# Performance work log

Measured on AMD Instinct MI355X. Metric: run time of the kernel, lower is better.

The kernel has to match this reference:

```python
import jax, jax.numpy as jnp
import numpy as np

B, TOK, D, H, L = 64, 20, 512, 8, 4
S = 512          # tokens per half
HD = D // H
ODIM = 32        # encoder_output_dim


def _ln(x, g, b):
    m = x.mean(-1, keepdims=True)
    v = ((x - m) ** 2).mean(-1, keepdims=True)
    return (x - m) / jnp.sqrt(v + 1e-5) * g + b


def _alibi_slopes(h):
    # mirrors FlashAttentionBlock.build_alibi_slopes (base=2.0)
    base = 2.0
    return jnp.asarray([1.0 / base ** (i // (h // base)) for i in range(h)], dtype=jnp.float32)


def setup_inputs() -> dict:
    key = jax.random.key(0)
    ks = jax.random.split(key, 16)
    r = lambda i, shape, s=0.02: jax.random.normal(ks[i], shape, jnp.float32) * s
    return {
        'x': jax.random.normal(ks[0], (B, 2 * S * TOK), jnp.float32),
        'in_W': r(1, (TOK, D)), 'in_b': jnp.zeros((D,)),
        'qkv_W': r(2, (L, D, 3 * D)), 'qkv_b': jnp.zeros((L, 3 * D)),
        'ln1_g': jnp.ones((L, D)), 'ln1_b': jnp.zeros((L, D)),
        'ffn_W1': r(3, (L, D, 4 * D)), 'ffn_b1': jnp.zeros((L, 4 * D)),
        'ffn_W2': r(4, (L, 4 * D, D)), 'ffn_b2': jnp.zeros((L, D)),
        'ln2_g': jnp.ones((L, D)), 'ln2_b': jnp.zeros((L, D)),
        'out_W': r(5, (D, ODIM)), 'out_b': jnp.zeros((ODIM,)),
        'd1_W': r(6, (2 * S * ODIM, 256)), 'd1_b': jnp.zeros((256,)),
        'bn1_g': jnp.ones((256,)), 'bn1_b': jnp.zeros((256,)),
        'bn1_m': jnp.zeros((256,)), 'bn1_v': jnp.ones((256,)),
        'd2_W': r(7, (256, 128)), 'd2_b': jnp.zeros((128,)),
        'bn2_g': jnp.ones((128,)), 'bn2_b': jnp.zeros((128,)),
        'bn2_m': jnp.zeros((128,)), 'bn2_v': jnp.ones((128,)),
        'fin_W': r(8, (128, 1)), 'fin_b': jnp.zeros((1,)),
    }


def _forward(x, in_W, in_b, qkv_W, qkv_b, ln1_g, ln1_b, ffn_W1, ffn_b1,
             ffn_W2, ffn_b2, ln2_g, ln2_b, out_W, out_b,
             d1_W, d1_b, bn1_g, bn1_b, bn1_m, bn1_v,
             d2_W, d2_b, bn2_g, bn2_b, bn2_m, bn2_v, fin_W, fin_b):
    slopes = _alibi_slopes(H)                                   # [H]
    pos = jnp.arange(S)
    # non-causal ALiBi bias: -slope * |i - j|, shape [H, S, S]
    bias = -slopes[:, None, None] * jnp.abs(pos[:, None] - pos[None, :]).astype(jnp.float32)
    scale = 1.0 / np.sqrt(HD).astype(np.float32)

    def encode(xh):
        b = xh.shape[0]
        t = xh.reshape(b, S, TOK) @ in_W + in_b                 # [b, S, D]
        for l in range(L):
            res = t
            qkv = (t @ qkv_W[l] + qkv_b[l]).reshape(b, S, 3, H, HD)
            q, k, v = qkv[:, :, 0], qkv[:, :, 1], qkv[:, :, 2]  # [b, S, H, HD]
            scores = jnp.einsum('bqhd,bkhd->bhqk', q, k) * scale + bias[None]
            attn = jax.nn.softmax(scores, axis=-1)
            o = jnp.einsum('bhqk,bkhd->bqhd', attn, v).reshape(b, S, D)
            t = _ln(res + o, ln1_g[l], ln1_b[l])
            res = t
            f = jax.nn.relu(t @ ffn_W1[l] + ffn_b1[l]) @ ffn_W2[l] + ffn_b2[l]
            t = _ln(res + f, ln2_g[l], ln2_b[l])
        return (t @ out_W + out_b).reshape(b, -1)               # [b, S*ODIM]

    half = S * TOK
    h = jnp.concatenate([encode(x[:, :half]), encode(x[:, half:])], axis=-1)
    bn = lambda z, g, bb, m, v: (z - m) / jnp.sqrt(v + 1e-5) * g + bb
    h = bn(jax.nn.relu(h @ d1_W + d1_b), bn1_g, bn1_b, bn1_m, bn1_v)
    h = bn(jax.nn.relu(h @ d2_W + d2_b), bn2_g, bn2_b, bn2_m, bn2_v)
    return (h @ fin_W + fin_b).squeeze(-1)                      # [B]


def reference(x, in_W, in_b, qkv_W, qkv_b, ln1_g, ln1_b, ffn_W1, ffn_b1,
              ffn_W2, ffn_b2, ln2_g, ln2_b, out_W, out_b,
              d1_W, d1_b, bn1_g, bn1_b, bn1_m, bn1_v,
              d2_W, d2_b, bn2_g, bn2_b, bn2_m, bn2_v, fin_W, fin_b):
    return _forward(x, in_W, in_b, qkv_W, qkv_b, ln1_g, ln1_b, ffn_W1, ffn_b1,
                    ffn_W2, ffn_b2, ln2_g, ln2_b, out_W, out_b,
                    d1_W, d1_b, bn1_g, bn1_b, bn1_m, bn1_v,
                    d2_W, d2_b, bn2_g, bn2_b, bn2_m, bn2_v, fin_W, fin_b)
```

## Files before the change

kernel.cpp:

```cpp
#include <hip/hip_runtime.h>

#define DEV __device__ __forceinline__

using bf16x8 = __attribute__((ext_vector_type(8))) __bf16;
using f32x4  = __attribute__((ext_vector_type(4))) float;
using u16x8  = __attribute__((ext_vector_type(8))) unsigned short;
using u16x4  = __attribute__((ext_vector_type(4))) unsigned short;

DEV unsigned short f2bf(float f) {
  unsigned u = __builtin_bit_cast(unsigned, f);
  u += 0x7fffu + ((u >> 16) & 1u);
  return (unsigned short)(u >> 16);
}
DEV float bf2f(unsigned short h) {
  unsigned u = ((unsigned)h) << 16;
  return __builtin_bit_cast(float, u);
}
DEV f32x4 mfma16(u16x8 a, u16x8 b, f32x4 c) {
  return __builtin_amdgcn_mfma_f32_16x16x32_bf16(
      __builtin_bit_cast(bf16x8, a), __builtin_bit_cast(bf16x8, b), c, 0, 0, 0);
}
DEV f32x4 zero4() { f32x4 z = {0.f, 0.f, 0.f, 0.f}; return z; }

DEV void glds16(const unsigned short* g, unsigned short* l) {
  __builtin_amdgcn_global_load_lds(
      (const __attribute__((address_space(1))) unsigned int*)g,
      (__attribute__((address_space(3))) unsigned int*)l, 16, 0, 0);
}

enum { EPI_BIAS = 0, EPI_RELU = 1, EPI_OUT = 2 };

template <int EPI>
__global__ __launch_bounds__(512, 2) void gemm256_k(
    const unsigned short* __restrict__ A, const unsigned short* __restrict__ Bt,
    const float* __restrict__ bias, unsigned short* __restrict__ C, int N, int K) {
  __shared__ unsigned short As[2][8192];
  __shared__ unsigned short Bs[2][8192];
  const int tid = threadIdx.x;
  const int lane = tid & 63, wv = tid >> 6;
  const int q = lane >> 4, ln = lane & 15;
  const int wr = wv >> 2, wc = wv & 3;

  const int Nt = gridDim.x, Mt = gridDim.y;
  const int lin = blockIdx.x + Nt * blockIdx.y;
  const int xcd = lin & 7;
  const int j = lin >> 3;
  const int mi = xcd * (Mt >> 3) + j / Nt;
  const int ni = j % Nt;
  const int m0 = mi << 8, n0 = ni << 8;

  f32x4 acc[8][4];
#pragma unroll
  for (int i = 0; i < 8; ++i)
#pragma unroll
    for (int jj = 0; jj < 4; ++jj) acc[i][jj] = zero4();

  const int srow = wv * 16 + (lane >> 2);
  const int scol = (((lane & 3) ^ ((lane >> 3) & 3)) << 3);
  const unsigned short* Ap = A + (size_t)(m0 + srow) * K + scol;
  const unsigned short* Bp = Bt + (size_t)(n0 + srow) * K + scol;

  auto STAGE = [&](int buf, int kb) {
    unsigned short* ab = &As[buf][wv * 512];
    unsigned short* bb = &Bs[buf][wv * 512];
    glds16(Ap + kb, ab);
    glds16(Ap + (size_t)128 * K + kb, ab + 4096);
    glds16(Bp + kb, bb);
    glds16(Bp + (size_t)128 * K + kb, bb + 4096);
  };

  const int sw = ((q ^ ((ln >> 1) & 3)) << 3);
  const int NTt = K >> 5;

  STAGE(0, 0);
  if (NTt > 1) {
    STAGE(1, 32);
    asm volatile("s_waitcnt vmcnt(4)" ::: "memory");
  } else {
    asm volatile("s_waitcnt vmcnt(0)" ::: "memory");
  }
  __builtin_amdgcn_sched_barrier(0);
  __builtin_amdgcn_s_barrier();
  __builtin_amdgcn_sched_barrier(0);

  for (int t = 0; t < NTt; ++t) {
    const int cur = t & 1;
    u16x8 af[4], bf[4], ag[4];
#pragma unroll
    for (int mt = 0; mt < 4; ++mt)
      af[mt] = *(const u16x8*)(&As[cur][(wr * 128 + mt * 16 + ln) * 32 + sw]);
#pragma unroll
    for (int nt = 0; nt < 4; ++nt)
      bf[nt] = *(const u16x8*)(&Bs[cur][(wc * 64 + nt * 16 + ln) * 32 + sw]);
    __builtin_amdgcn_s_setprio(1);
#pragma unroll
    for (int nt = 0; nt < 4; ++nt)
#pragma unroll
      for (int mt = 0; mt < 4; ++mt) acc[mt][nt] = mfma16(af[mt], bf[nt], acc[mt][nt]);
    __builtin_amdgcn_s_setprio(0);
#pragma unroll
    for (int mt = 0; mt < 4; ++mt)
      ag[mt] = *(const u16x8*)(&As[cur][(wr * 128 + (mt + 4) * 16 + ln) * 32 + sw]);
    asm volatile("s_waitcnt lgkmcnt(0)" ::: "memory");
    __builtin_amdgcn_sched_barrier(0);
    __builtin_amdgcn_s_barrier();
    __builtin_amdgcn_sched_barrier(0);
    if (t + 2 < NTt) STAGE(cur, (t + 2) * 32);
    __builtin_amdgcn_s_setprio(1);
#pragma unroll
    for (int nt = 0; nt < 4; ++nt)
#pragma unroll
      for (int mt = 0; mt < 4; ++mt)
        acc[mt + 4][nt] = mfma16(ag[mt], bf[nt], acc[mt + 4][nt]);
    __builtin_amdgcn_s_setprio(0);
    if (t < NTt - 1) {
      if (t + 2 < NTt) {
        asm volatile("s_waitcnt vmcnt(4)" ::: "memory");
      } else {
        asm volatile("s_waitcnt vmcnt(0)" ::: "memory");
      }
      __builtin_amdgcn_sched_barrier(0);
      __builtin_amdgcn_s_barrier();
      __builtin_amdgcn_sched_barrier(0);
    }
  }

#pragma unroll
  for (int mt = 0; mt < 8; ++mt) {
    const int rowb = m0 + wr * 128 + mt * 16 + q * 4;
#pragma unroll
    for (int nt = 0; nt < 4; ++nt) {
      const int col = n0 + wc * 64 + nt * 16 + ln;
      const float bs = bias[col];
#pragma unroll
      for (int r = 0; r < 4; ++r) {
        float v = acc[mt][nt][r] + bs;
        if (EPI == EPI_RELU) v = fmaxf(v, 0.f);
        C[(size_t)(rowb + r) * N + col] = f2bf(v);
      }
    }
  }
}

template <int EPI>
__global__ __launch_bounds__(256) void gemm_k(
    const unsigned short* __restrict__ A, const unsigned short* __restrict__ Bt,
    const float* __restrict__ bias, unsigned short* __restrict__ C, int N, int K) {
  __shared__ unsigned short As[128 * 64];
  __shared__ unsigned short Bs[128 * 64];
  const int tid = threadIdx.x;
  const int lane = tid & 63, wv = tid >> 6;
  const int q = lane >> 4, ln = lane & 15;
  const int wr = wv >> 1, wc = wv & 1;

  const int Nt = gridDim.x, Mt = gridDim.y;
  const int lin = blockIdx.x + Nt * blockIdx.y;
  const int xcd = lin & 7;
  const int j = lin >> 3;
  const int mi = xcd * (Mt >> 3) + j / Nt;
  const int ni = j % Nt;
  const int m0 = mi << 7, n0 = ni << 7;

  f32x4 acc[4][4];
#pragma unroll
  for (int i = 0; i < 4; ++i)
#pragma unroll
    for (int jj = 0; jj < 4; ++jj) acc[i][jj] = zero4();

  const int ra = lane >> 3;
  const int ca = ((lane & 7) ^ ra) << 3;
  const unsigned short* Ap = A + (size_t)(m0 + wv * 32 + ra) * K + ca;
  const unsigned short* Bp = Bt + (size_t)(n0 + wv * 32 + ra) * K + ca;
  unsigned short* AsW = As + wv * 2048;
  unsigned short* BsW = Bs + wv * 2048;
  const int ln7 = ln & 7;

  for (int kb = 0; kb < K; kb += 64) {
    __syncthreads();
#pragma unroll
    for (int t = 0; t < 4; ++t) {
      glds16(Ap + (size_t)(t * 8) * K + kb, AsW + t * 512);
      glds16(Bp + (size_t)(t * 8) * K + kb, BsW + t * 512);
    }
    __syncthreads();
#pragma unroll
    for (int kk = 0; kk < 2; ++kk) {
      const int c = kk * 4 + q;
      const int lo = ln * 64 + ((c ^ ln7) << 3);
      u16x8 af[4];
#pragma unroll
      for (int mt = 0; mt < 4; ++mt)
        af[mt] = *(const u16x8*)(As + (wr * 64 + mt * 16) * 64 + lo);
#pragma unroll
      for (int nt = 0; nt < 4; ++nt) {
        u16x8 bf = *(const u16x8*)(Bs + (wc * 64 + nt * 16) * 64 + lo);
#pragma unroll
        for (int mt = 0; mt < 4; ++mt) acc[mt][nt] = mfma16(af[mt], bf, acc[mt][nt]);
      }
    }
  }

#pragma unroll
  for (int mt = 0; mt < 4; ++mt) {
    const int rowb = m0 + wr * 64 + mt * 16 + q * 4;
#pragma unroll
    for (int nt = 0; nt < 4; ++nt) {
      const int col = n0 + wc * 64 + nt * 16 + ln;
      if (EPI == EPI_OUT && col >= 32) continue;
      const float bs = bias[col];
      const int ldc = (EPI == EPI_OUT) ? 32 : N;
#pragma unroll
      for (int r = 0; r < 4; ++r) {
        float v = acc[mt][nt][r] + bs;
        if (EPI == EPI_RELU) v = fmaxf(v, 0.f);
        C[(size_t)(rowb + r) * ldc + col] = f2bf(v);
      }
    }
  }
}

__global__ __launch_bounds__(256) void vt_k(const unsigned short* __restrict__ big,
                                            unsigned short* __restrict__ vt) {
  __shared__ unsigned short td[64 * 72];
  const int tid = threadIdx.x;
  const int sh = blockIdx.x;
  const int seq = sh >> 3, h = sh & 7;
  const int kt = blockIdx.y;
  {
    const int key = tid >> 2, hdc = (tid & 3) << 4;
    const unsigned short* src =
        big + ((size_t)seq * 512 + kt * 64 + key) * 1536 + 1024 + h * 64 + hdc;
    *(u16x8*)(td + key * 72 + hdc) = *(const u16x8*)src;
    *(u16x8*)(td + key * 72 + hdc + 8) = *(const u16x8*)(src + 8);
  }
  __syncthreads();
  {
    const int hd = tid >> 2, kc = (tid & 3) << 4;
    u16x8 a, b;
#pragma unroll
    for (int j = 0; j < 8; ++j) a[j] = td[(kc + j) * 72 + hd];
#pragma unroll
    for (int j = 0; j < 8; ++j) b[j] = td[(kc + 8 + j) * 72 + hd];
    unsigned short* dst = vt + ((size_t)sh * 64 + hd) * 512 + kt * 64 + kc;
    *(u16x8*)dst = a;
    *(u16x8*)(dst + 8) = b;
  }
}

__global__ __launch_bounds__(256) void attn_k(const unsigned short* __restrict__ qkv,
                                              const unsigned short* __restrict__ vt,
                                              unsigned short* __restrict__ o) {
  __shared__ unsigned short Qs[128 * 72];
  __shared__ unsigned short Ks[64 * 64];
  __shared__ unsigned short Vts[64 * 64];
  unsigned short* Ps = Qs;
  const int tid = threadIdx.x;
  const int lane = tid & 63, w = tid >> 6, q = lane >> 4, ln = lane & 15;
  const int bh = blockIdx.x;
  const int seq = bh >> 3, h = bh & 7;
  const int qt = blockIdx.y;
  const size_t tokb = (size_t)seq * 512;
  const int qoff = h * 64, koff = 512 + h * 64;
  const float c1 = 0.125f * 1.44269504f;
  const float c2 = ((h < 4) ? 1.0f : 0.5f) * 1.44269504f;

#pragma unroll
  for (int p = 0; p < 4; ++p) {
    int c = p * 256 + tid;
    int row = c >> 3, cc = (c & 7) << 3;
    u16x8 v = *(const u16x8*)(qkv + (tokb + qt * 128 + row) * 1536 + qoff + cc);
    *(u16x8*)(Qs + row * 72 + cc) = v;
  }
  __syncthreads();
  u16x8 aq[2][2];
#pragma unroll
  for (int mt = 0; mt < 2; ++mt)
#pragma unroll
    for (int kc = 0; kc < 2; ++kc)
      aq[mt][kc] = *(const u16x8*)(Qs + (w * 32 + mt * 16 + ln) * 72 + kc * 32 + q * 8);

  float lacc[2] = {0.f, 0.f};
  f32x4 o_acc[2][4];
#pragma unroll
  for (int mt = 0; mt < 2; ++mt)
#pragma unroll
    for (int ht = 0; ht < 4; ++ht) o_acc[mt][ht] = zero4();

  const int sr = lane >> 3;
  const int sc = ((lane & 7) ^ sr) << 3;
  const unsigned short* Kp = qkv + (tokb + w * 16 + sr) * 1536 + koff + sc;
  const unsigned short* Vp = vt + ((size_t)bh * 64 + w * 16 + sr) * 512 + sc;
  unsigned short* KsW = Ks + w * 1024;
  unsigned short* VsW = Vts + w * 1024;
  const int ln7 = ln & 7;

  for (int kt = 0; kt < 8; ++kt) {
    __syncthreads();
    glds16(Kp + (size_t)(kt * 64) * 1536, KsW);
    glds16(Kp + (size_t)(kt * 64 + 8) * 1536, KsW + 512);
    glds16(Vp + kt * 64, VsW);
    glds16(Vp + kt * 64 + (size_t)8 * 512, VsW + 512);
    __syncthreads();

    f32x4 sacc[2][4];
#pragma unroll
    for (int mt = 0; mt < 2; ++mt)
#pragma unroll
      for (int nt = 0; nt < 4; ++nt) sacc[mt][nt] = zero4();
#pragma unroll
    for (int nt = 0; nt < 4; ++nt)
#pragma unroll
      for (int kc = 0; kc < 2; ++kc) {
        u16x8 bk = *(const u16x8*)(Ks + (nt * 16 + ln) * 64 + (((kc * 4 + q) ^ ln7) << 3));
#pragma unroll
        for (int mt = 0; mt < 2; ++mt) sacc[mt][nt] = mfma16(bk, aq[mt][kc], sacc[mt][nt]);
      }

    const float qp0 = (float)(qt * 128 + w * 32 + ln);
    const float kb0 = (float)(kt * 64 + q * 4);
#pragma unroll
    for (int mt = 0; mt < 2; ++mt) {
      const float qpm = qp0 + (float)(mt * 16);
#pragma unroll
      for (int nt = 0; nt < 4; ++nt) {
        const float kp = kb0 + (float)(nt * 16);
        u16x4 pk;
#pragma unroll
        for (int r = 0; r < 4; ++r) {
          const float ad = fabsf(qpm - (kp + (float)r));
          const float p = exp2f(fmaf(sacc[mt][nt][r], c1, -c2 * ad));
          const unsigned u = __builtin_bit_cast(unsigned, p);
          const unsigned short pb = (unsigned short)((u + 0x8000u) >> 16);
          pk[r] = pb;
          lacc[mt] += bf2f(pb);
        }
        *(u16x4*)(Ps + (w * 32 + mt * 16 + ln) * 72 + nt * 16 + q * 4) = pk;
      }
    }
#pragma unroll
    for (int kc = 0; kc < 2; ++kc) {
      u16x8 pa[2];
#pragma unroll
      for (int mt = 0; mt < 2; ++mt)
        pa[mt] = *(const u16x8*)(Ps + (w * 32 + mt * 16 + ln) * 72 + kc * 32 + q * 8);
#pragma unroll
      for (int ht = 0; ht < 4; ++ht) {
        u16x8 bv = *(const u16x8*)(Vts + (ht * 16 + ln) * 64 + (((kc * 4 + q) ^ ln7) << 3));
#pragma unroll
        for (int mt = 0; mt < 2; ++mt) o_acc[mt][ht] = mfma16(pa[mt], bv, o_acc[mt][ht]);
      }
    }
  }

  float rl[2][4];
#pragma unroll
  for (int mt = 0; mt < 2; ++mt) {
    float l = lacc[mt];
    l += __shfl_xor(l, 16, 64);
    l += __shfl_xor(l, 32, 64);
    const int sb = (lane >> 4) * 20;
#pragma unroll
    for (int r = 0; r < 4; ++r) rl[mt][r] = 1.0f / __shfl(l, sb + r, 64);
  }

#pragma unroll
  for (int mt = 0; mt < 2; ++mt)
#pragma unroll
    for (int ht = 0; ht < 4; ++ht)
#pragma unroll
      for (int r = 0; r < 4; ++r) {
        const int row = qt * 128 + w * 32 + mt * 16 + q * 4 + r;
        const float val = o_acc[mt][ht][r] * rl[mt][r];
        o[(tokb + row) * 512 + h * 64 + ht * 16 + ln] = f2bf(val);
      }
}

__global__ __launch_bounds__(256) void ln_k(const unsigned short* res,
                                            const unsigned short* __restrict__ y,
                                            const float* __restrict__ g,
                                            const float* __restrict__ b,
                                            unsigned short* out) {
  const int lane = threadIdx.x & 63, wv = threadIdx.x >> 6;
  const size_t row = (size_t)blockIdx.x * 4 + wv;
  const size_t base = row * 512 + lane * 8;
  u16x8 rv = *(const u16x8*)(res + base);
  u16x8 yv = *(const u16x8*)(y + base);
  float v[8];
  float s = 0.f, s2 = 0.f;
#pragma unroll
  for (int i = 0; i < 8; ++i) {
    v[i] = bf2f(rv[i]) + bf2f(yv[i]);
    s += v[i];
    s2 += v[i] * v[i];
  }
#pragma unroll
  for (int m = 1; m < 64; m <<= 1) {
    s += __shfl_xor(s, m, 64);
    s2 += __shfl_xor(s2, m, 64);
  }
  const float mean = s * (1.f / 512.f);
  const float var = s2 * (1.f / 512.f) - mean * mean;
  const float rstd = rsqrtf(var + 1e-5f);
  const int c = lane * 8;
  u16x8 ov;
#pragma unroll
  for (int i = 0; i < 8; ++i) ov[i] = f2bf((v[i] - mean) * rstd * g[c + i] + b[c + i]);
  *(u16x8*)(out + base) = ov;
}

__global__ __launch_bounds__(256) void transpose_w(const float* __restrict__ in,
                                                   unsigned short* __restrict__ out,
                                                   int Kin, int Nin, int Kout, int Nout) {
  __shared__ float tile[32][33];
  const int nb = blockIdx.x * 32, kb = blockIdx.y * 32;
  const int tx = threadIdx.x & 31, ty = threadIdx.x >> 5;
#pragma unroll
  for (int i = 0; i < 32; i += 8) {
    int k = kb + ty + i, n = nb + tx;
    tile[ty + i][tx] = (k < Kin && n < Nin) ? in[(size_t)k * Nin + n] : 0.f;
  }
  __syncthreads();
#pragma unroll
  for (int i = 0; i < 32; i += 8) {
    int n = nb + ty + i, k = kb + tx;
    if (n < Nout && k < Kout) out[(size_t)n * Kout + k] = f2bf(tile[tx][ty + i]);
  }
}

__global__ __launch_bounds__(256) void xpad_k(const float* __restrict__ x,
                                              unsigned short* __restrict__ xp) {
  const int idx = blockIdx.x * 256 + threadIdx.x;
  const int tok = idx >> 6, k = idx & 63;
  const int seq = tok >> 9, s = tok & 511;
  const int hf = seq >> 6, b = seq & 63;
  float v = 0.f;
  if (k < 20) v = x[(size_t)b * 20480 + hf * 10240 + s * 20 + k];
  xp[idx] = f2bf(v);
}

__global__ __launch_bounds__(256) void d1_part(const unsigned short* __restrict__ enc,
                                               const float* __restrict__ W,
                                               float* __restrict__ pz) {
  __shared__ float ef[64 * 128];
  const int tid = threadIdx.x;
  const int kb = blockIdx.x * 128;
  const int hf = kb >> 14;
  const int j0 = kb & 16383;
  {
    const int m = tid >> 2, c = (tid & 3) * 32;
    const unsigned short* src = enc + (size_t)hf * 1048576 + (size_t)m * 16384 + j0 + c;
#pragma unroll
    for (int i = 0; i < 4; ++i) {
      u16x8 v = *(const u16x8*)(src + i * 8);
#pragma unroll
      for (int jj = 0; jj < 8; ++jj) ef[m * 128 + c + i * 8 + jj] = bf2f(v[jj]);
    }
  }
  __syncthreads();
  const int n = tid;
  float acc[64];
#pragma unroll
  for (int m = 0; m < 64; ++m) acc[m] = 0.f;
  for (int kc = 0; kc < 128; kc += 4) {
    const float w0 = W[(size_t)(kb + kc) * 256 + n];
    const float w1 = W[(size_t)(kb + kc + 1) * 256 + n];
    const float w2 = W[(size_t)(kb + kc + 2) * 256 + n];
    const float w3 = W[(size_t)(kb + kc + 3) * 256 + n];
#pragma unroll
    for (int m = 0; m < 64; ++m) {
      const f32x4 e = *(const f32x4*)(ef + m * 128 + kc);
      acc[m] += e[0] * w0 + e[1] * w1 + e[2] * w2 + e[3] * w3;
    }
  }
#pragma unroll
  for (int m = 0; m < 64; ++m)
    pz[(size_t)(blockIdx.x * 64 + m) * 256 + n] = acc[m];
}

__global__ __launch_bounds__(256) void d1_fin(const float* __restrict__ pz,
                                              const float* __restrict__ d1b,
                                              const float* __restrict__ g,
                                              const float* __restrict__ b,
                                              const float* __restrict__ mm,
                                              const float* __restrict__ vv,
                                              float* __restrict__ h1) {
  const int m = blockIdx.x, n = threadIdx.x;
  float a = d1b[n];
  for (int sl = 0; sl < 256; ++sl) a += pz[(size_t)(sl * 64 + m) * 256 + n];
  a = fmaxf(a, 0.f);
  a = (a - mm[n]) * rsqrtf(vv[n] + 1e-5f) * g[n] + b[n];
  h1[m * 256 + n] = a;
}

__global__ __launch_bounds__(128) void d2_k(const float* __restrict__ h1,
                                            const float* __restrict__ W,
                                            const float* __restrict__ bb,
                                            const float* __restrict__ g,
                                            const float* __restrict__ b,
                                            const float* __restrict__ mm,
                                            const float* __restrict__ vv,
                                            float* __restrict__ h2) {
  __shared__ float hs[256];
  const int m = blockIdx.x, n = threadIdx.x;
  hs[n] = h1[m * 256 + n];
  hs[n + 128] = h1[m * 256 + n + 128];
  __syncthreads();
  float a = bb[n];
#pragma unroll 8
  for (int k = 0; k < 256; ++k) a += hs[k] * W[k * 128 + n];
  a = fmaxf(a, 0.f);
  a = (a - mm[n]) * rsqrtf(vv[n] + 1e-5f) * g[n] + b[n];
  h2[m * 128 + n] = a;
}

__global__ __launch_bounds__(64) void fin_k(const float* __restrict__ h2,
                                            const float* __restrict__ W,
                                            const float* __restrict__ fb,
                                            float* __restrict__ out) {
  const int m = threadIdx.x;
  float a = fb[0];
#pragma unroll 8
  for (int k = 0; k < 128; ++k) a += h2[m * 128 + k] * W[k];
  out[m] = a;
}

extern "C" void kernel_launch(void* const* d_in, const int* in_sizes, int n_in,
                              void* d_out, int out_size, void* d_ws, size_t ws_size,
                              hipStream_t stream) {
  const float* x      = (const float*)d_in[0];
  const float* in_W   = (const float*)d_in[1];
  const float* in_b   = (const float*)d_in[2];
  const float* qkv_W  = (const float*)d_in[3];
  const float* qkv_b  = (const float*)d_in[4];
  const float* ln1_g  = (const float*)d_in[5];
  const float* ln1_b  = (const float*)d_in[6];
  const float* ffn_W1 = (const float*)d_in[7];
  const float* ffn_b1 = (const float*)d_in[8];
  const float* ffn_W2 = (const float*)d_in[9];
  const float* ffn_b2 = (const float*)d_in[10];
  const float* ln2_g  = (const float*)d_in[11];
  const float* ln2_b  = (const float*)d_in[12];
  const float* out_W  = (const float*)d_in[13];
  const float* out_b  = (const float*)d_in[14];
  const float* d1W    = (const float*)d_in[15];
  const float* d1b    = (const float*)d_in[16];
  const float* bn1g   = (const float*)d_in[17];
  const float* bn1b   = (const float*)d_in[18];
  const float* bn1m   = (const float*)d_in[19];
  const float* bn1v   = (const float*)d_in[20];
  const float* d2W    = (const float*)d_in[21];
  const float* d2b    = (const float*)d_in[22];
  const float* bn2g   = (const float*)d_in[23];
  const float* bn2b   = (const float*)d_in[24];
  const float* bn2m   = (const float*)d_in[25];
  const float* bn2v   = (const float*)d_in[26];
  const float* finW   = (const float*)d_in[27];
  const float* finb   = (const float*)d_in[28];
  (void)in_sizes; (void)n_in; (void)out_size; (void)ws_size;

  char* ws = (char*)d_ws;
  size_t off = 0;
  auto alloc = [&](size_t bytes) {
    char* p = ws + off;
    off += (bytes + 255) & ~(size_t)255;
    return p;
  };
  unsigned short* t     = (unsigned short*)alloc(32768ull * 512 * 2);
  unsigned short* big   = (unsigned short*)alloc(32768ull * 2048 * 2);
  unsigned short* ob    = (unsigned short*)alloc(32768ull * 512 * 2);
  unsigned short* xpad  = (unsigned short*)alloc(65536ull * 64 * 2);
  unsigned short* enc   = (unsigned short*)alloc(65536ull * 32 * 2);
  unsigned short* inWt  = (unsigned short*)alloc(512ull * 64 * 2);
  unsigned short* qkvWt = (unsigned short*)alloc(4ull * 1536 * 512 * 2);
  unsigned short* f1Wt  = (unsigned short*)alloc(4ull * 2048 * 512 * 2);
  unsigned short* f2Wt  = (unsigned short*)alloc(4ull * 512 * 2048 * 2);
  unsigned short* outWt = (unsigned short*)alloc(128ull * 512 * 2);
  float* h1 = (float*)alloc(64ull * 256 * 4);
  float* h2 = (float*)alloc(64ull * 128 * 4);
  float* pz = (float*)big;
  unsigned short* vtb = big + (size_t)32768 * 1536;

  xpad_k<<<16384, 256, 0, stream>>>(x, xpad);
  transpose_w<<<dim3(16, 2), 256, 0, stream>>>(in_W, inWt, 20, 512, 64, 512);
  transpose_w<<<dim3(4, 16), 256, 0, stream>>>(out_W, outWt, 512, 32, 512, 128);
  for (int l = 0; l < 4; ++l) {
    transpose_w<<<dim3(48, 16), 256, 0, stream>>>(qkv_W + (size_t)l * 512 * 1536,
                                                  qkvWt + (size_t)l * 1536 * 512, 512, 1536, 512, 1536);
    transpose_w<<<dim3(64, 16), 256, 0, stream>>>(ffn_W1 + (size_t)l * 512 * 2048,
                                                  f1Wt + (size_t)l * 2048 * 512, 512, 2048, 512, 2048);
    transpose_w<<<dim3(16, 64), 256, 0, stream>>>(ffn_W2 + (size_t)l * 2048 * 512,
                                                  f2Wt + (size_t)l * 512 * 2048, 2048, 512, 2048, 512);
  }

  for (int hf = 0; hf < 2; ++hf) {
    gemm256_k<EPI_BIAS><<<dim3(2, 128), 512, 0, stream>>>(xpad + (size_t)hf * 32768 * 64, inWt, in_b, t, 512, 64);
    for (int l = 0; l < 4; ++l) {
      gemm256_k<EPI_BIAS><<<dim3(6, 128), 512, 0, stream>>>(t, qkvWt + (size_t)l * 1536 * 512,
                                                            qkv_b + l * 1536, big, 1536, 512);
      vt_k<<<dim3(512, 8), 256, 0, stream>>>(big, vtb);
      attn_k<<<dim3(512, 4), 256, 0, stream>>>(big, vtb, ob);
      ln_k<<<8192, 256, 0, stream>>>(t, ob, ln1_g + l * 512, ln1_b + l * 512, t);
      gemm256_k<EPI_RELU><<<dim3(8, 128), 512, 0, stream>>>(t, f1Wt + (size_t)l * 2048 * 512,
                                                            ffn_b1 + l * 2048, big, 2048, 512);
      gemm256_k<EPI_BIAS><<<dim3(2, 128), 512, 0, stream>>>(big, f2Wt + (size_t)l * 512 * 2048,
                                                            ffn_b2 + l * 512, ob, 512, 2048);
      ln_k<<<8192, 256, 0, stream>>>(t, ob, ln2_g + l * 512, ln2_b + l * 512, t);
    }
    gemm_k<EPI_OUT><<<dim3(1, 256), 256, 0, stream>>>(t, outWt, out_b,
                                                      enc + (size_t)hf * 32768 * 32, 128, 512);
  }

  d1_part<<<256, 256, 0, stream>>>(enc, d1W, pz);
  d1_fin<<<64, 256, 0, stream>>>(pz, d1b, bn1g, bn1b, bn1m, bn1v, h1);
  d2_k<<<64, 128, 0, stream>>>(h1, d2W, d2b, bn2g, bn2b, bn2m, bn2v, h2);
  fin_k<<<1, 64, 0, stream>>>(h2, finW, finb, (float*)d_out);
}
```

Before: 3.226 ms.

## Restructure 256x256 GEMM into 8-phase schedule with 64-wide K tiles

Replaces the 256x256 bf16 GEMM main loop with a version that loads 64-wide K tiles into doubled LDS buffers, using an 8-column XOR swizzle. Each K step is split into four MFMA quadrants, and the global-to-LDS loads for the next tiles are interleaved between them, separated by barriers. The goal is to overlap memory traffic with MFMA work and halve the number of loop iterations. In exchange, LDS use doubles, which drops the kernel to one block per CU, and each iteration now has more barriers.

```diff
diff --git a/kernel.cpp b/kernel.cpp
--- a/kernel.cpp
+++ b/kernel.cpp
@@ -28,18 +28,26 @@
       (__attribute__((address_space(3))) unsigned int*)l, 16, 0, 0);
 }
 
+#define PH_BAR()                          \
+  do {                                    \
+    __builtin_amdgcn_sched_barrier(0);    \
+    __builtin_amdgcn_s_barrier();         \
+    __builtin_amdgcn_sched_barrier(0);    \
+  } while (0)
+
 enum { EPI_BIAS = 0, EPI_RELU = 1, EPI_OUT = 2 };
 
 template <int EPI>
-__global__ __launch_bounds__(512, 2) void gemm256_k(
+__global__ __launch_bounds__(512, 1) void gemm8p_k(
     const unsigned short* __restrict__ A, const unsigned short* __restrict__ Bt,
     const float* __restrict__ bias, unsigned short* __restrict__ C, int N, int K) {
-  __shared__ unsigned short As[2][8192];
-  __shared__ unsigned short Bs[2][8192];
+  __shared__ unsigned short As[2][16384];
+  __shared__ unsigned short Bs[2][16384];
   const int tid = threadIdx.x;
   const int lane = tid & 63, wv = tid >> 6;
   const int q = lane >> 4, ln = lane & 15;
   const int wr = wv >> 2, wc = wv & 3;
+  const int ln7 = ln & 7;
 
   const int Nt = gridDim.x, Mt = gridDim.y;
   const int lin = blockIdx.x + Nt * blockIdx.y;
@@ -55,73 +63,126 @@
 #pragma unroll
     for (int jj = 0; jj < 4; ++jj) acc[i][jj] = zero4();
 
-  const int srow = wv * 16 + (lane >> 2);
-  const int scol = (((lane & 3) ^ ((lane >> 3) & 3)) << 3);
-  const unsigned short* Ap = A + (size_t)(m0 + srow) * K + scol;
-  const unsigned short* Bp = Bt + (size_t)(n0 + srow) * K + scol;
-
-  auto STAGE = [&](int buf, int kb) {
-    unsigned short* ab = &As[buf][wv * 512];
-    unsigned short* bb = &Bs[buf][wv * 512];
-    glds16(Ap + kb, ab);
-    glds16(Ap + (size_t)128 * K + kb, ab + 4096);
-    glds16(Bp + kb, bb);
-    glds16(Bp + (size_t)128 * K + kb, bb + 4096);
+  const int sr = lane >> 3;
+  const int sc = ((lane & 7) ^ sr) << 3;
+  const unsigned short* Abase = A + (size_t)(m0 + wv * 8 + sr) * K + sc;
+  const unsigned short* Bbase = Bt + (size_t)(n0 + wv * 8 + sr) * K + sc;
+
+  const int T = K >> 6;
+
+  auto stA = [&](int buf, int t, int half) {
+    unsigned short* d = &As[buf][(half * 128 + wv * 8) * 64];
+    const unsigned short* s = Abase + (size_t)(half * 128) * K + t * 64;
+    glds16(s, d);
+    glds16(s + (size_t)64 * K, d + 4096);
   };
-
-  const int sw = ((q ^ ((ln >> 1) & 3)) << 3);
-  const int NTt = K >> 5;
-
-  STAGE(0, 0);
-  if (NTt > 1) {
-    STAGE(1, 32);
+  auto stB = [&](int buf, int t, int half) {
+    unsigned short* d = &Bs[buf][(half * 128 + wv * 8) * 64];
+    const unsigned short* s = Bbase + (size_t)(half * 128) * K + t * 64;
+    glds16(s, d);
+    glds16(s + (size_t)64 * K, d + 4096);
+  };
+
+  stB(0, 0, 0);
+  stB(0, 0, 1);
+  stA(0, 0, 0);
+  stA(0, 0, 1);
+  if (T > 1) {
+    stB(1, 1, 0);
+    stB(1, 1, 1);
     asm volatile("s_waitcnt vmcnt(4)" ::: "memory");
   } else {
     asm volatile("s_waitcnt vmcnt(0)" ::: "memory");
   }
-  __builtin_amdgcn_sched_barrier(0);
-  __builtin_amdgcn_s_barrier();
-  __builtin_amdgcn_sched_barrier(0);
-
-  for (int t = 0; t < NTt; ++t) {
-    const int cur = t & 1;
-    u16x8 af[4], bf[4], ag[4];
+  PH_BAR();
+
+  for (int u = 0; u < T; ++u) {
+    const int cur = u & 1, nxt = cur ^ 1;
+    const unsigned short* Ab = &As[cur][0];
+    const unsigned short* Bb = &Bs[cur][0];
+    u16x8 a0[4][2], a1[4][2], b0[2][2], b1[2][2];
+
 #pragma unroll
     for (int mt = 0; mt < 4; ++mt)
-      af[mt] = *(const u16x8*)(&As[cur][(wr * 128 + mt * 16 + ln) * 32 + sw]);
-#pragma unroll
-    for (int nt = 0; nt < 4; ++nt)
-      bf[nt] = *(const u16x8*)(&Bs[cur][(wc * 64 + nt * 16 + ln) * 32 + sw]);
+#pragma unroll
+      for (int kk = 0; kk < 2; ++kk)
+        a0[mt][kk] = *(const u16x8*)(Ab + (wr * 128 + mt * 16 + ln) * 64 +
+                                     (((kk * 4 + q) ^ ln7) << 3));
+#pragma unroll
+    for (int nt = 0; nt < 2; ++nt)
+#pragma unroll
+      for (int kk = 0; kk < 2; ++kk)
+        b0[nt][kk] = *(const u16x8*)(Bb + (wc * 64 + nt * 16 + ln) * 64 +
+                                     (((kk * 4 + q) ^ ln7) << 3));
+    if (u + 1 < T) stA(nxt, u + 1, 0);
+    PH_BAR();
     __builtin_amdgcn_s_setprio(1);
 #pragma unroll
-    for (int nt = 0; nt < 4; ++nt)
-#pragma unroll
-      for (int mt = 0; mt < 4; ++mt) acc[mt][nt] = mfma16(af[mt], bf[nt], acc[mt][nt]);
+    for (int kk = 0; kk < 2; ++kk)
+#pragma unroll
+      for (int nt = 0; nt < 2; ++nt)
+#pragma unroll
+        for (int mt = 0; mt < 4; ++mt)
+          acc[mt][nt] = mfma16(a0[mt][kk], b0[nt][kk], acc[mt][nt]);
     __builtin_amdgcn_s_setprio(0);
+    PH_BAR();
+
+#pragma unroll
+    for (int nt = 0; nt < 2; ++nt)
+#pragma unroll
+      for (int kk = 0; kk < 2; ++kk)
+        b1[nt][kk] = *(const u16x8*)(Bb + (wc * 64 + (nt + 2) * 16 + ln) * 64 +
+                                     (((kk * 4 + q) ^ ln7) << 3));
+    if (u + 1 < T) stA(nxt, u + 1, 1);
+    PH_BAR();
+    __builtin_amdgcn_s_setprio(1);
+#pragma unroll
+    for (int kk = 0; kk < 2; ++kk)
+#pragma unroll
+      for (int nt = 0; nt < 2; ++nt)
+#pragma unroll
+        for (int mt = 0; mt < 4; ++mt)
+          acc[mt][nt + 2] = mfma16(a0[mt][kk], b1[nt][kk], acc[mt][nt + 2]);
+    __builtin_amdgcn_s_setprio(0);
+    PH_BAR();
+
 #pragma unroll
     for (int mt = 0; mt < 4; ++mt)
-      ag[mt] = *(const u16x8*)(&As[cur][(wr * 128 + (mt + 4) * 16 + ln) * 32 + sw]);
-    asm volatile("s_waitcnt lgkmcnt(0)" ::: "memory");
-    __builtin_amdgcn_sched_barrier(0);
-    __builtin_amdgcn_s_barrier();
-    __builtin_amdgcn_sched_barrier(0);
-    if (t + 2 < NTt) STAGE(cur, (t + 2) * 32);
+#pragma unroll
+      for (int kk = 0; kk < 2; ++kk)
+        a1[mt][kk] = *(const u16x8*)(Ab + (wr * 128 + (mt + 4) * 16 + ln) * 64 +
+                                     (((kk * 4 + q) ^ ln7) << 3));
+    if (u + 2 < T) stB(cur, u + 2, 0);
+    PH_BAR();
     __builtin_amdgcn_s_setprio(1);
 #pragma unroll
-    for (int nt = 0; nt < 4; ++nt)
-#pragma unroll
-      for (int mt = 0; mt < 4; ++mt)
-        acc[mt + 4][nt] = mfma16(ag[mt], bf[nt], acc[mt + 4][nt]);
+    for (int kk = 0; kk < 2; ++kk)
+#pragma unroll
+      for (int nt = 0; nt < 2; ++nt)
+#pragma unroll
+        for (int mt = 0; mt < 4; ++mt)
+          acc[mt + 4][nt] = mfma16(a1[mt][kk], b0[nt][kk], acc[mt + 4][nt]);
     __builtin_amdgcn_s_setprio(0);
-    if (t < NTt - 1) {
-      if (t + 2 < NTt) {
+    PH_BAR();
+
+    if (u + 2 < T) stB(cur, u + 2, 1);
+    PH_BAR();
+    __builtin_amdgcn_s_setprio(1);
+#pragma unroll
+    for (int kk = 0; kk < 2; ++kk)
+#pragma unroll
+      for (int nt = 0; nt < 2; ++nt)
+#pragma unroll
+        for (int mt = 0; mt < 4; ++mt)
+          acc[mt + 4][nt + 2] = mfma16(a1[mt][kk], b1[nt][kk], acc[mt + 4][nt + 2]);
+    __builtin_amdgcn_s_setprio(0);
+    if (u + 1 < T) {
+      if (u + 2 < T) {
         asm volatile("s_waitcnt vmcnt(4)" ::: "memory");
       } else {
         asm volatile("s_waitcnt vmcnt(0)" ::: "memory");
       }
-      __builtin_amdgcn_sched_barrier(0);
-      __builtin_amdgcn_s_barrier();
-      __builtin_amdgcn_sched_barrier(0);
+      PH_BAR();
     }
   }
 
@@ -593,17 +654,17 @@
   }
 
   for (int hf = 0; hf < 2; ++hf) {
-    gemm256_k<EPI_BIAS><<<dim3(2, 128), 512, 0, stream>>>(xpad + (size_t)hf * 32768 * 64, inWt, in_b, t, 512, 64);
+    gemm8p_k<EPI_BIAS><<<dim3(2, 128), 512, 0, stream>>>(xpad + (size_t)hf * 32768 * 64, inWt, in_b, t, 512, 64);
     for (int l = 0; l < 4; ++l) {
-      gemm256_k<EPI_BIAS><<<dim3(6, 128), 512, 0, stream>>>(t, qkvWt + (size_t)l * 1536 * 512,
-                                                            qkv_b + l * 1536, big, 1536, 512);
+      gemm8p_k<EPI_BIAS><<<dim3(6, 128), 512, 0, stream>>>(t, qkvWt + (size_t)l * 1536 * 512,
+                                                           qkv_b + l * 1536, big, 1536, 512);
       vt_k<<<dim3(512, 8), 256, 0, stream>>>(big, vtb);
       attn_k<<<dim3(512, 4), 256, 0, stream>>>(big, vtb, ob);
       ln_k<<<8192, 256, 0, stream>>>(t, ob, ln1_g + l * 512, ln1_b + l * 512, t);
-      gemm256_k<EPI_RELU><<<dim3(8, 128), 512, 0, stream>>>(t, f1Wt + (size_t)l * 2048 * 512,
-                                                            ffn_b1 + l * 2048, big, 2048, 512);
-      gemm256_k<EPI_BIAS><<<dim3(2, 128), 512, 0, stream>>>(big, f2Wt + (size_t)l * 512 * 2048,
-                                                            ffn_b2 + l * 512, ob, 512, 2048);
+      gemm8p_k<EPI_RELU><<<dim3(8, 128), 512, 0, stream>>>(t, f1Wt + (size_t)l * 2048 * 512,
+                                                           ffn_b1 + l * 2048, big, 2048, 512);
+      gemm8p_k<EPI_BIAS><<<dim3(2, 128), 512, 0, stream>>>(big, f2Wt + (size_t)l * 512 * 2048,
+                                                           ffn_b2 + l * 512, ob, 512, 2048);
       ln_k<<<8192, 256, 0, stream>>>(t, ob, ln2_g + l * 512, ln2_b + l * 512, t);
     }
     gemm_k<EPI_OUT><<<dim3(1, 256), 256, 0, stream>>>(t, outWt, out_b,
```

Result: faster. 2.998 ms (-7.1%).

## Re-phase GEMM main loop and double-buffer K/V tiles in attention

Applied to the files above, without the earlier changes.

The 256x256 GEMM loop is split into phases separated by workgroup barriers. B tile prefetch is issued during the second MFMA half and A tile prefetch after it, and the LDS read swizzle is changed to q^(ln&3). The attention kernel gains double-buffered K and V LDS tiles, so the next tile's global-to-LDS load is issued before the current tile is computed, overlapping memory with MFMA. The extra barriers may add synchronisation overhead, and the doubled LDS in attention may reduce occupancy.

```diff
diff --git a/kernel.cpp b/kernel.cpp
--- a/kernel.cpp
+++ b/kernel.cpp
@@ -28,10 +28,17 @@
       (__attribute__((address_space(3))) unsigned int*)l, 16, 0, 0);
 }
 
+#define PH_BAR()                          \
+  do {                                    \
+    __builtin_amdgcn_sched_barrier(0);    \
+    __builtin_amdgcn_s_barrier();         \
+    __builtin_amdgcn_sched_barrier(0);    \
+  } while (0)
+
 enum { EPI_BIAS = 0, EPI_RELU = 1, EPI_OUT = 2 };
 
 template <int EPI>
-__global__ __launch_bounds__(512, 2) void gemm256_k(
+__global__ __launch_bounds__(512, 2) void gemm32_k(
     const unsigned short* __restrict__ A, const unsigned short* __restrict__ Bt,
     const float* __restrict__ bias, unsigned short* __restrict__ C, int N, int K) {
   __shared__ unsigned short As[2][8192];
@@ -40,6 +47,7 @@
   const int lane = tid & 63, wv = tid >> 6;
   const int q = lane >> 4, ln = lane & 15;
   const int wr = wv >> 2, wc = wv & 3;
+  const int ln3 = ln & 3;
 
   const int Nt = gridDim.x, Mt = gridDim.y;
   const int lin = blockIdx.x + Nt * blockIdx.y;
@@ -55,73 +63,80 @@
 #pragma unroll
     for (int jj = 0; jj < 4; ++jj) acc[i][jj] = zero4();
 
-  const int srow = wv * 16 + (lane >> 2);
-  const int scol = (((lane & 3) ^ ((lane >> 3) & 3)) << 3);
-  const unsigned short* Ap = A + (size_t)(m0 + srow) * K + scol;
-  const unsigned short* Bp = Bt + (size_t)(n0 + srow) * K + scol;
-
-  auto STAGE = [&](int buf, int kb) {
-    unsigned short* ab = &As[buf][wv * 512];
-    unsigned short* bb = &Bs[buf][wv * 512];
-    glds16(Ap + kb, ab);
-    glds16(Ap + (size_t)128 * K + kb, ab + 4096);
-    glds16(Bp + kb, bb);
-    glds16(Bp + (size_t)128 * K + kb, bb + 4096);
+  const int sr = lane >> 2;
+  const int sc = ((lane & 3) ^ (sr & 3)) << 3;
+  const unsigned short* Abase = A + (size_t)(m0 + wv * 16 + sr) * K + sc;
+  const unsigned short* Bbase = Bt + (size_t)(n0 + wv * 16 + sr) * K + sc;
+
+  const int T = K >> 5;
+
+  auto stA = [&](int buf, int t) {
+    unsigned short* d = &As[buf][wv * 512];
+    const unsigned short* s = Abase + t * 32;
+    glds16(s, d);
+    glds16(s + (size_t)128 * K, d + 4096);
   };
-
-  const int sw = ((q ^ ((ln >> 1) & 3)) << 3);
-  const int NTt = K >> 5;
-
-  STAGE(0, 0);
-  if (NTt > 1) {
-    STAGE(1, 32);
+  auto stB = [&](int buf, int t) {
+    unsigned short* d = &Bs[buf][wv * 512];
+    const unsigned short* s = Bbase + t * 32;
+    glds16(s, d);
+    glds16(s + (size_t)128 * K, d + 4096);
+  };
+
+  stA(0, 0);
+  stB(0, 0);
+  if (T > 1) {
+    stA(1, 1);
+    stB(1, 1);
     asm volatile("s_waitcnt vmcnt(4)" ::: "memory");
   } else {
     asm volatile("s_waitcnt vmcnt(0)" ::: "memory");
   }
-  __builtin_amdgcn_sched_barrier(0);
-  __builtin_amdgcn_s_barrier();
-  __builtin_amdgcn_sched_barrier(0);
-
-  for (int t = 0; t < NTt; ++t) {
-    const int cur = t & 1;
-    u16x8 af[4], bf[4], ag[4];
+  PH_BAR();
+
+  for (int u = 0; u < T; ++u) {
+    const int cur = u & 1;
+    const unsigned short* Ab = &As[cur][0];
+    const unsigned short* Bb = &Bs[cur][0];
+    u16x8 a0[4], a1[4], b0[4];
+
 #pragma unroll
     for (int mt = 0; mt < 4; ++mt)
-      af[mt] = *(const u16x8*)(&As[cur][(wr * 128 + mt * 16 + ln) * 32 + sw]);
+      a0[mt] = *(const u16x8*)(Ab + (wr * 128 + mt * 16 + ln) * 32 + ((q ^ ln3) << 3));
 #pragma unroll
     for (int nt = 0; nt < 4; ++nt)
-      bf[nt] = *(const u16x8*)(&Bs[cur][(wc * 64 + nt * 16 + ln) * 32 + sw]);
+      b0[nt] = *(const u16x8*)(Bb + (wc * 64 + nt * 16 + ln) * 32 + ((q ^ ln3) << 3));
+    PH_BAR();
     __builtin_amdgcn_s_setprio(1);
 #pragma unroll
     for (int nt = 0; nt < 4; ++nt)
 #pragma unroll
-      for (int mt = 0; mt < 4; ++mt) acc[mt][nt] = mfma16(af[mt], bf[nt], acc[mt][nt]);
+      for (int mt = 0; mt < 4; ++mt) acc[mt][nt] = mfma16(a0[mt], b0[nt], acc[mt][nt]);
     __builtin_amdgcn_s_setprio(0);
+    PH_BAR();
+
 #pragma unroll
     for (int mt = 0; mt < 4; ++mt)
-      ag[mt] = *(const u16x8*)(&As[cur][(wr * 128 + (mt + 4) * 16 + ln) * 32 + sw]);
-    asm volatile("s_waitcnt lgkmcnt(0)" ::: "memory");
-    __builtin_amdgcn_sched_barrier(0);
-    __builtin_amdgcn_s_barrier();
-    __builtin_amdgcn_sched_barrier(0);
-    if (t + 2 < NTt) STAGE(cur, (t + 2) * 32);
+      a1[mt] = *(const u16x8*)(Ab + (wr * 128 + (mt + 4) * 16 + ln) * 32 + ((q ^ ln3) << 3));
+    if (u + 2 < T) stB(cur, u + 2);
+    PH_BAR();
     __builtin_amdgcn_s_setprio(1);
 #pragma unroll
     for (int nt = 0; nt < 4; ++nt)
 #pragma unroll
       for (int mt = 0; mt < 4; ++mt)
-        acc[mt + 4][nt] = mfma16(ag[mt], bf[nt], acc[mt + 4][nt]);
+        acc[mt + 4][nt] = mfma16(a1[mt], b0[nt], acc[mt + 4][nt]);
     __builtin_amdgcn_s_setprio(0);
-    if (t < NTt - 1) {
-      if (t + 2 < NTt) {
+    PH_BAR();
+
+    if (u + 1 < T) {
+      if (u + 2 < T) {
+        stA(cur, u + 2);
         asm volatile("s_waitcnt vmcnt(4)" ::: "memory");
       } else {
         asm volatile("s_waitcnt vmcnt(0)" ::: "memory");
       }
-      __builtin_amdgcn_sched_barrier(0);
-      __builtin_amdgcn_s_barrier();
-      __builtin_amdgcn_sched_barrier(0);
+      PH_BAR();
     }
   }
 
@@ -251,8 +266,8 @@
                                               const unsigned short* __restrict__ vt,
                                               unsigned short* __restrict__ o) {
   __shared__ unsigned short Qs[128 * 72];
-  __shared__ unsigned short Ks[64 * 64];
-  __shared__ unsigned short Vts[64 * 64];
+  __shared__ unsigned short Ks[2][64 * 64];
+  __shared__ unsigned short Vts[2][64 * 64];
   unsigned short* Ps = Qs;
   const int tid = threadIdx.x;
   const int lane = tid & 63, w = tid >> 6, q = lane >> 4, ln = lane & 15;
@@ -271,36 +286,51 @@
     u16x8 v = *(const u16x8*)(qkv + (tokb + qt * 128 + row) * 1536 + qoff + cc);
     *(u16x8*)(Qs + row * 72 + cc) = v;
   }
-  __syncthreads();
-  u16x8 aq[2][2];
-#pragma unroll
-  for (int mt = 0; mt < 2; ++mt)
-#pragma unroll
-    for (int kc = 0; kc < 2; ++kc)
-      aq[mt][kc] = *(const u16x8*)(Qs + (w * 32 + mt * 16 + ln) * 72 + kc * 32 + q * 8);
-
-  float lacc[2] = {0.f, 0.f};
-  f32x4 o_acc[2][4];
-#pragma unroll
-  for (int mt = 0; mt < 2; ++mt)
-#pragma unroll
-    for (int ht = 0; ht < 4; ++ht) o_acc[mt][ht] = zero4();
 
   const int sr = lane >> 3;
   const int sc = ((lane & 7) ^ sr) << 3;
   const unsigned short* Kp = qkv + (tokb + w * 16 + sr) * 1536 + koff + sc;
   const unsigned short* Vp = vt + ((size_t)bh * 64 + w * 16 + sr) * 512 + sc;
-  unsigned short* KsW = Ks + w * 1024;
-  unsigned short* VsW = Vts + w * 1024;
   const int ln7 = ln & 7;
 
-  for (int kt = 0; kt < 8; ++kt) {
-    __syncthreads();
+  auto stage = [&](int kt, int buf) {
+    unsigned short* KsW = &Ks[buf][w * 1024];
+    unsigned short* VsW = &Vts[buf][w * 1024];
     glds16(Kp + (size_t)(kt * 64) * 1536, KsW);
     glds16(Kp + (size_t)(kt * 64 + 8) * 1536, KsW + 512);
     glds16(Vp + kt * 64, VsW);
     glds16(Vp + kt * 64 + (size_t)8 * 512, VsW + 512);
+  };
+
+  stage(0, 0);
+
+  __syncthreads();
+  u16x8 aq[2][2];
+#pragma unroll
+  for (int mt = 0; mt < 2; ++mt)
+#pragma unroll
+    for (int kc = 0; kc < 2; ++kc)
+      aq[mt][kc] = *(const u16x8*)(Qs + (w * 32 + mt * 16 + ln) * 72 + kc * 32 + q * 8);
+
+  float lacc[2] = {0.f, 0.f};
+  f32x4 o_acc[2][4];
+#pragma unroll
+  for (int mt = 0; mt < 2; ++mt)
+#pragma unroll
+    for (int ht = 0; ht < 4; ++ht) o_acc[mt][ht] = zero4();
+
+  for (int kt = 0; kt < 8; ++kt) {
+    const int buf = kt & 1;
     __syncthreads();
+    if (kt + 1 < 8) {
+      stage(kt + 1, buf ^ 1);
+      asm volatile("s_waitcnt vmcnt(4)" ::: "memory");
+    } else {
+      asm volatile("s_waitcnt vmcnt(0)" ::: "memory");
+    }
+    __builtin_amdgcn_sched_barrier(0);
+    __builtin_amdgcn_s_barrier();
+    __builtin_amdgcn_sched_barrier(0);
 
     f32x4 sacc[2][4];
 #pragma unroll
@@ -311,7 +341,7 @@
     for (int nt = 0; nt < 4; ++nt)
 #pragma unroll
       for (int kc = 0; kc < 2; ++kc) {
-        u16x8 bk = *(const u16x8*)(Ks + (nt * 16 + ln) * 64 + (((kc * 4 + q) ^ ln7) << 3));
+        u16x8 bk = *(const u16x8*)(&Ks[buf][(nt * 16 + ln) * 64 + (((kc * 4 + q) ^ ln7) << 3)]);
 #pragma unroll
         for (int mt = 0; mt < 2; ++mt) sacc[mt][nt] = mfma16(bk, aq[mt][kc], sacc[mt][nt]);
       }
@@ -345,7 +375,7 @@
         pa[mt] = *(const u16x8*)(Ps + (w * 32 + mt * 16 + ln) * 72 + kc * 32 + q * 8);
 #pragma unroll
       for (int ht = 0; ht < 4; ++ht) {
-        u16x8 bv = *(const u16x8*)(Vts + (ht * 16 + ln) * 64 + (((kc * 4 + q) ^ ln7) << 3));
+        u16x8 bv = *(const u16x8*)(&Vts[buf][(ht * 16 + ln) * 64 + (((kc * 4 + q) ^ ln7) << 3)]);
 #pragma unroll
         for (int mt = 0; mt < 2; ++mt) o_acc[mt][ht] = mfma16(pa[mt], bv, o_acc[mt][ht]);
       }
@@ -593,17 +623,17 @@
   }
 
   for (int hf = 0; hf < 2; ++hf) {
-    gemm256_k<EPI_BIAS><<<dim3(2, 128), 512, 0, stream>>>(xpad + (size_t)hf * 32768 * 64, inWt, in_b, t, 512, 64);
+    gemm32_k<EPI_BIAS><<<dim3(2, 128), 512, 0, stream>>>(xpad + (size_t)hf * 32768 * 64, inWt, in_b, t, 512, 64);
     for (int l = 0; l < 4; ++l) {
-      gemm256_k<EPI_BIAS><<<dim3(6, 128), 512, 0, stream>>>(t, qkvWt + (size_t)l * 1536 * 512,
-                                                            qkv_b + l * 1536, big, 1536, 512);
+      gemm32_k<EPI_BIAS><<<dim3(6, 128), 512, 0, stream>>>(t, qkvWt + (size_t)l * 1536 * 512,
+                                                           qkv_b + l * 1536, big, 1536, 512);
       vt_k<<<dim3(512, 8), 256, 0, stream>>>(big, vtb);
       attn_k<<<dim3(512, 4), 256, 0, stream>>>(big, vtb, ob);
       ln_k<<<8192, 256, 0, stream>>>(t, ob, ln1_g + l * 512, ln1_b + l * 512, t);
-      gemm256_k<EPI_RELU><<<dim3(8, 128), 512, 0, stream>>>(t, f1Wt + (size_t)l * 2048 * 512,
-                                                            ffn_b1 + l * 2048, big, 2048, 512);
-      gemm256_k<EPI_BIAS><<<dim3(2, 128), 512, 0, stream>>>(big, f2Wt + (size_t)l * 512 * 2048,
-                                                            ffn_b2 + l * 512, ob, 512, 2048);
+      gemm32_k<EPI_RELU><<<dim3(8, 128), 512, 0, stream>>>(t, f1Wt + (size_t)l * 2048 * 512,
+                                                           ffn_b1 + l * 2048, big, 2048, 512);
+      gemm32_k<EPI_BIAS><<<dim3(2, 128), 512, 0, stream>>>(big, f2Wt + (size_t)l * 512 * 2048,
+                                                           ffn_b2 + l * 512, ob, 512, 2048);
       ln_k<<<8192, 256, 0, stream>>>(t, ob, ln2_g + l * 512, ln2_b + l * 512, t);
     }
     gemm_k<EPI_OUT><<<dim3(1, 256), 256, 0, stream>>>(t, outWt, out_b,
```

Result: slower. 3.364 ms (+4.3%).
